# Kernel tuning notes

Hardware: AMD Instinct MI355X
Metric: run time of the kernel (lower is better)

## Reference

```python
import math
import jax, jax.numpy as jnp
import numpy as np

D_MODEL = 1024
D_STATE = 16
DT_MIN, DT_MAX, DT_INIT_FLOOR = 1e-3, 1e-1, 1e-4


def setup_inputs() -> dict:
    key = jax.random.key(0)
    ks = jax.random.split(key, 7)
    B, L, D, N = 2, 2048, D_MODEL, D_STATE
    hidden_states = jax.random.normal(ks[0], (B, L, D), dtype=jnp.float32)
    # dt init: exp(U*(log dt_max - log dt_min) + log dt_min), clamped, then log
    u = jax.random.uniform(ks[1], (D,), dtype=jnp.float32)
    dt = jnp.clip(jnp.exp(u * (math.log(DT_MAX) - math.log(DT_MIN)) + math.log(DT_MIN)), DT_INIT_FLOOR, None)
    log_dt = jnp.log(dt)
    A_real_log = jnp.log(0.5 * jnp.ones((D, N), dtype=jnp.float32))
    A_imag = jnp.broadcast_to(math.pi * jnp.arange(1, N + 1, dtype=jnp.float32)[None, :], (D, N)).copy()
    # xavier_normal std for (D, N)
    std = math.sqrt(2.0 / (D + N))
    B_re = std * jax.random.normal(ks[2], (D, N), dtype=jnp.float32)
    B_im = std * jax.random.normal(ks[3], (D, N), dtype=jnp.float32)
    C_re = std * jax.random.normal(ks[4], (D, N), dtype=jnp.float32)
    C_im = std * jax.random.normal(ks[5], (D, N), dtype=jnp.float32)
    Dparam = jnp.ones((D,), dtype=jnp.float32)
    return {"hidden_states": hidden_states, "log_dt": log_dt, "A_real_log": A_real_log,
            "A_imag": A_imag, "B_re": B_re, "B_im": B_im, "C_re": C_re, "C_im": C_im,
            "Dparam": Dparam}


def reference(hidden_states, log_dt, A_real_log, A_imag, B_re, B_im, C_re, C_im, Dparam):
    # hidden_states: (B, L, D)
    Bsz, L, Dm = hidden_states.shape
    A = -jnp.exp(A_real_log) + 1j * A_imag              # (D, N) complex64
    dt = jnp.exp(log_dt)                                 # (D,), broadcast over (B, L)
    delta = jax.nn.softplus(dt)                          # delta_softplus=True
    dA = jnp.exp(delta[:, None] * A)                     # (D, N) time-invariant discretized A
    Bc = B_re + 1j * B_im                                # (D, N)
    Cc = C_re + 1j * C_im                                # (D, N)
    dB = (delta[:, None] * Bc)                           # (D, N)

    xs = jnp.transpose(hidden_states, (1, 0, 2))         # (L, B, D)
    h0 = jnp.zeros((Bsz, Dm, A.shape[1]), dtype=A.dtype)

    def step(h, xt):
        # h: (B, D, N) complex; xt: (B, D) real
        h = dA[None] * h + dB[None] * xt[..., None].astype(h.dtype)
        y = 2.0 * jnp.real(jnp.einsum('bdn,dn->bd', h, Cc))  # complex C/B => 2*real
        return h, y

    _, ys = jax.lax.scan(step, h0, xs)                   # ys: (L, B, D)
    out = jnp.transpose(ys, (1, 0, 2)) + hidden_states * Dparam[None, None, :]
    return out
```

## Files before the change

### kernel.cpp

```cpp
#include <hip/hip_runtime.h>
#include <math.h>

namespace {
constexpr int kB = 2;
constexpr int kL = 2048;
constexpr int kD = 1024;
constexpr int kN = 16;
constexpr int kChunk = 32;
constexpr int kNC = kL / kChunk;
constexpr int kW = 24;
}

typedef float f2 __attribute__((ext_vector_type(2)));

__device__ __forceinline__ float s4_delta(float log_dt) {
  return log1pf(expf(expf(log_dt)));
}

__device__ __forceinline__ f2 s4_step(f2 g, f2 arr, f2 amp, f2 x2) {
  f2 gs = __builtin_shufflevector(g, g, 1, 0);
  f2 t = __builtin_elementwise_fma(arr, g, x2);
  return __builtin_elementwise_fma(amp, gs, t);
}

__global__ __launch_bounds__(64) void s4_window(
    const float* __restrict__ X, const float* __restrict__ log_dt,
    const float* __restrict__ A_real_log, const float* __restrict__ A_imag,
    const float* __restrict__ B_re, const float* __restrict__ B_im,
    const float* __restrict__ C_re, const float* __restrict__ C_im,
    const float* __restrict__ Dparam, float* __restrict__ Y)
{
  const int lane = threadIdx.x;
  const int bid = blockIdx.x;
  const int dblk = bid & 15;
  const int c = (bid >> 4) & (kNC - 1);
  const int b = bid >> 10;
  const int d = dblk * 64 + lane;

  const size_t base = ((size_t)b * kL + (size_t)c * kChunk) * kD + d;
  const float* xp = X + base;

  float xw[kW];
  float xo[kChunk];
  if (c > 0) {
    #pragma unroll
    for (int i = 0; i < kW; ++i) xw[i] = xp[(ptrdiff_t)(i - kW) * kD];
  }
  #pragma unroll
  for (int i = 0; i < kChunk; ++i) xo[i] = xp[(size_t)i * kD];

  const float delta = s4_delta(log_dt[d]);

  f2 arr[kN], amp[kN], cb[kN];
  {
    const float4* arl4 = reinterpret_cast<const float4*>(A_real_log + (size_t)d * kN);
    const float4* ai4  = reinterpret_cast<const float4*>(A_imag + (size_t)d * kN);
    const float4* br4  = reinterpret_cast<const float4*>(B_re + (size_t)d * kN);
    const float4* bi4  = reinterpret_cast<const float4*>(B_im + (size_t)d * kN);
    const float4* cr4  = reinterpret_cast<const float4*>(C_re + (size_t)d * kN);
    const float4* ci4  = reinterpret_cast<const float4*>(C_im + (size_t)d * kN);
    #pragma unroll
    for (int q = 0; q < 4; ++q) {
      float4 a = arl4[q];
      float4 im = ai4[q];
      float4 br = br4[q];
      float4 bi = bi4[q];
      float4 cr = cr4[q];
      float4 ci = ci4[q];
      float av[4] = {a.x, a.y, a.z, a.w};
      float iv[4] = {im.x, im.y, im.z, im.w};
      float brv[4] = {br.x, br.y, br.z, br.w};
      float biv[4] = {bi.x, bi.y, bi.z, bi.w};
      float crv[4] = {cr.x, cr.y, cr.z, cr.w};
      float civ[4] = {ci.x, ci.y, ci.z, ci.w};
      #pragma unroll
      for (int j = 0; j < 4; ++j) {
        const int n = q * 4 + j;
        float mag = expf(-delta * expf(av[j]));
        float ph = delta * iv[j];
        float are = mag * cosf(ph);
        float aim = mag * sinf(ph);
        arr[n] = (f2){are, are};
        amp[n] = (f2){-aim, aim};
        float dbre = delta * brv[j];
        float dbim = delta * biv[j];
        float cbre = 2.f * (crv[j] * dbre - civ[j] * dbim);
        float cbim = 2.f * (crv[j] * dbim + civ[j] * dbre);
        cb[n] = (f2){cbre, -cbim};
      }
    }
  }
  const float Dd = Dparam[d];

  f2 g[kN];
  #pragma unroll
  for (int n = 0; n < kN; ++n) g[n] = (f2){0.f, 0.f};

  if (c > 0) {
    #pragma unroll
    for (int t = 0; t < kW; ++t) {
      const f2 x2 = (f2){xw[t], 0.f};
      #pragma unroll
      for (int n = 0; n < kN; ++n) g[n] = s4_step(g[n], arr[n], amp[n], x2);
    }
  }

  float* yp = Y + base;
  #pragma unroll
  for (int t = 0; t < kChunk; ++t) {
    const float x = xo[t];
    const f2 x2 = (f2){x, 0.f};
    f2 ya0 = (f2){x * Dd, 0.f};
    f2 ya1 = (f2){0.f, 0.f}, ya2 = (f2){0.f, 0.f}, ya3 = (f2){0.f, 0.f};
    #pragma unroll
    for (int n = 0; n < kN; ++n) {
      g[n] = s4_step(g[n], arr[n], amp[n], x2);
      if ((n & 3) == 0)      ya0 = __builtin_elementwise_fma(cb[n], g[n], ya0);
      else if ((n & 3) == 1) ya1 = __builtin_elementwise_fma(cb[n], g[n], ya1);
      else if ((n & 3) == 2) ya2 = __builtin_elementwise_fma(cb[n], g[n], ya2);
      else                   ya3 = __builtin_elementwise_fma(cb[n], g[n], ya3);
    }
    const f2 ys = (ya0 + ya1) + (ya2 + ya3);
    yp[(size_t)t * kD] = ys.x + ys.y;
  }
}

extern "C" void kernel_launch(void* const* d_in, const int* in_sizes, int n_in,
                              void* d_out, int out_size, void* d_ws, size_t ws_size,
                              hipStream_t stream) {
  const float* X          = (const float*)d_in[0];
  const float* log_dt     = (const float*)d_in[1];
  const float* A_real_log = (const float*)d_in[2];
  const float* A_imag     = (const float*)d_in[3];
  const float* B_re       = (const float*)d_in[4];
  const float* B_im       = (const float*)d_in[5];
  const float* C_re       = (const float*)d_in[6];
  const float* C_im       = (const float*)d_in[7];
  const float* Dparam     = (const float*)d_in[8];
  float* Y = (float*)d_out;

  const int nblk = kB * kNC * (kD / 64);
  s4_window<<<nblk, 64, 0, stream>>>(X, log_dt, A_real_log, A_imag,
                                     B_re, B_im, C_re, C_im, Dparam, Y);
}
```

Baseline: 102.4 us.

## Stage input chunk with warmup window in LDS via float4 loads, double chunk length

Measured after the change: 105.8 us. +3.4%, slower.

```diff
diff --git a/kernel.cpp b/kernel.cpp
--- a/kernel.cpp
+++ b/kernel.cpp
@@ -6,9 +6,12 @@
 constexpr int kL = 2048;
 constexpr int kD = 1024;
 constexpr int kN = 16;
-constexpr int kChunk = 32;
+constexpr int kChunk = 64;
 constexpr int kNC = kL / kChunk;
 constexpr int kW = 24;
+constexpr int kDQ = 8;
+constexpr int kSlice = kD / kDQ;
+constexpr int kRows = kChunk + kW;
 }
 
 typedef float f2 __attribute__((ext_vector_type(2)));
@@ -23,31 +26,38 @@
   return __builtin_elementwise_fma(amp, gs, t);
 }
 
-__global__ __launch_bounds__(64) void s4_window(
+__global__ __launch_bounds__(128) void s4_lds(
     const float* __restrict__ X, const float* __restrict__ log_dt,
     const float* __restrict__ A_real_log, const float* __restrict__ A_imag,
     const float* __restrict__ B_re, const float* __restrict__ B_im,
     const float* __restrict__ C_re, const float* __restrict__ C_im,
     const float* __restrict__ Dparam, float* __restrict__ Y)
 {
-  const int lane = threadIdx.x;
+  __shared__ float sx[kRows * kSlice];
+
+  const int tid = threadIdx.x;
   const int bid = blockIdx.x;
-  const int dblk = bid & 15;
-  const int c = (bid >> 4) & (kNC - 1);
-  const int b = bid >> 10;
-  const int d = dblk * 64 + lane;
+  const int dq = bid & 7;
+  const int c = (bid >> 3) & (kNC - 1);
+  const int b = bid >> 8;
+  const int d = dq * kSlice + tid;
 
-  const size_t base = ((size_t)b * kL + (size_t)c * kChunk) * kD + d;
-  const float* xp = X + base;
-
-  float xw[kW];
-  float xo[kChunk];
-  if (c > 0) {
-    #pragma unroll
-    for (int i = 0; i < kW; ++i) xw[i] = xp[(ptrdiff_t)(i - kW) * kD];
+  const int woff = (c > 0) ? kW : 0;
+  const int nrows = kChunk + woff;
+  const int slot0 = kW - woff;
+  {
+    const size_t gbase = ((size_t)b * kL + (size_t)(c * kChunk - woff)) * kD
+                         + (size_t)dq * kSlice;
+    float4* s4v = reinterpret_cast<float4*>(sx);
+    const int n4 = nrows * (kSlice / 4);
+    #pragma unroll 4
+    for (int i = tid; i < n4; i += 128) {
+      const int r = i >> 5;
+      const int j = i & 31;
+      const float4* src = reinterpret_cast<const float4*>(X + gbase + (size_t)r * kD);
+      s4v[(slot0 + r) * (kSlice / 4) + j] = src[j];
+    }
   }
-  #pragma unroll
-  for (int i = 0; i < kChunk; ++i) xo[i] = xp[(size_t)i * kD];
 
   const float delta = s4_delta(log_dt[d]);
 
@@ -92,36 +102,48 @@
   }
   const float Dd = Dparam[d];
 
+  __syncthreads();
+
   f2 g[kN];
   #pragma unroll
   for (int n = 0; n < kN; ++n) g[n] = (f2){0.f, 0.f};
 
   if (c > 0) {
-    #pragma unroll
-    for (int t = 0; t < kW; ++t) {
-      const f2 x2 = (f2){xw[t], 0.f};
+    for (int tt = 0; tt < kW; tt += 8) {
+      float xg[8];
       #pragma unroll
-      for (int n = 0; n < kN; ++n) g[n] = s4_step(g[n], arr[n], amp[n], x2);
+      for (int j = 0; j < 8; ++j) xg[j] = sx[(tt + j) * kSlice + tid];
+      #pragma unroll
+      for (int j = 0; j < 8; ++j) {
+        const f2 x2 = (f2){xg[j], 0.f};
+        #pragma unroll
+        for (int n = 0; n < kN; ++n) g[n] = s4_step(g[n], arr[n], amp[n], x2);
+      }
     }
   }
 
-  float* yp = Y + base;
-  #pragma unroll
-  for (int t = 0; t < kChunk; ++t) {
-    const float x = xo[t];
-    const f2 x2 = (f2){x, 0.f};
-    f2 ya0 = (f2){x * Dd, 0.f};
-    f2 ya1 = (f2){0.f, 0.f}, ya2 = (f2){0.f, 0.f}, ya3 = (f2){0.f, 0.f};
+  float* yp = Y + ((size_t)b * kL + (size_t)c * kChunk) * kD + d;
+  for (int tt = 0; tt < kChunk; tt += 8) {
+    float xg[8];
     #pragma unroll
-    for (int n = 0; n < kN; ++n) {
-      g[n] = s4_step(g[n], arr[n], amp[n], x2);
-      if ((n & 3) == 0)      ya0 = __builtin_elementwise_fma(cb[n], g[n], ya0);
-      else if ((n & 3) == 1) ya1 = __builtin_elementwise_fma(cb[n], g[n], ya1);
-      else if ((n & 3) == 2) ya2 = __builtin_elementwise_fma(cb[n], g[n], ya2);
-      else                   ya3 = __builtin_elementwise_fma(cb[n], g[n], ya3);
+    for (int j = 0; j < 8; ++j) xg[j] = sx[(kW + tt + j) * kSlice + tid];
+    #pragma unroll
+    for (int j = 0; j < 8; ++j) {
+      const float x = xg[j];
+      const f2 x2 = (f2){x, 0.f};
+      f2 ya0 = (f2){x * Dd, 0.f};
+      f2 ya1 = (f2){0.f, 0.f}, ya2 = (f2){0.f, 0.f}, ya3 = (f2){0.f, 0.f};
+      #pragma unroll
+      for (int n = 0; n < kN; ++n) {
+        g[n] = s4_step(g[n], arr[n], amp[n], x2);
+        if ((n & 3) == 0)      ya0 = __builtin_elementwise_fma(cb[n], g[n], ya0);
+        else if ((n & 3) == 1) ya1 = __builtin_elementwise_fma(cb[n], g[n], ya1);
+        else if ((n & 3) == 2) ya2 = __builtin_elementwise_fma(cb[n], g[n], ya2);
+        else                   ya3 = __builtin_elementwise_fma(cb[n], g[n], ya3);
+      }
+      const f2 ys = (ya0 + ya1) + (ya2 + ya3);
+      yp[(size_t)(tt + j) * kD] = ys.x + ys.y;
     }
-    const f2 ys = (ya0 + ya1) + (ya2 + ya3);
-    yp[(size_t)t * kD] = ys.x + ys.y;
   }
 }
 
@@ -139,7 +161,7 @@
   const float* Dparam     = (const float*)d_in[8];
   float* Y = (float*)d_out;
 
-  const int nblk = kB * kNC * (kD / 64);
-  s4_window<<<nblk, 64, 0, stream>>>(X, log_dt, A_real_log, A_imag,
-                                     B_re, B_im, C_re, C_im, Dparam, Y);
+  const int nblk = kB * kNC * kDQ;
+  s4_lds<<<nblk, 128, 0, stream>>>(X, log_dt, A_real_log, A_imag,
+                                   B_re, B_im, C_re, C_im, Dparam, Y);
 }
```

## Replace windowed complex recurrence with precomputed 24-tap FIR convolution

Applied to the files above, without the earlier changes.

After: 92.05 us (median of 2 runs). 10.1% less time.

```diff
diff --git a/kernel.cpp b/kernel.cpp
--- a/kernel.cpp
+++ b/kernel.cpp
@@ -6,122 +6,110 @@
 constexpr int kL = 2048;
 constexpr int kD = 1024;
 constexpr int kN = 16;
-constexpr int kChunk = 32;
-constexpr int kNC = kL / kChunk;
-constexpr int kW = 24;
+constexpr int kK = 24;
+constexpr int kT = 32;
+constexpr int kHalo = kK - 1;
 }
-
-typedef float f2 __attribute__((ext_vector_type(2)));
 
 __device__ __forceinline__ float s4_delta(float log_dt) {
   return log1pf(expf(expf(log_dt)));
 }
 
-__device__ __forceinline__ f2 s4_step(f2 g, f2 arr, f2 amp, f2 x2) {
-  f2 gs = __builtin_shufflevector(g, g, 1, 0);
-  f2 t = __builtin_elementwise_fma(arr, g, x2);
-  return __builtin_elementwise_fma(amp, gs, t);
-}
-
-__global__ __launch_bounds__(64) void s4_window(
-    const float* __restrict__ X, const float* __restrict__ log_dt,
+__global__ __launch_bounds__(256) void s4_taps(
+    const float* __restrict__ log_dt,
     const float* __restrict__ A_real_log, const float* __restrict__ A_imag,
     const float* __restrict__ B_re, const float* __restrict__ B_im,
     const float* __restrict__ C_re, const float* __restrict__ C_im,
-    const float* __restrict__ Dparam, float* __restrict__ Y)
+    const float* __restrict__ Dparam, float* __restrict__ H)
 {
-  const int lane = threadIdx.x;
-  const int bid = blockIdx.x;
-  const int dblk = bid & 15;
-  const int c = (bid >> 4) & (kNC - 1);
-  const int b = bid >> 10;
-  const int d = dblk * 64 + lane;
-
-  const size_t base = ((size_t)b * kL + (size_t)c * kChunk) * kD + d;
-  const float* xp = X + base;
-
-  float xw[kW];
-  float xo[kChunk];
-  if (c > 0) {
-    #pragma unroll
-    for (int i = 0; i < kW; ++i) xw[i] = xp[(ptrdiff_t)(i - kW) * kD];
-  }
-  #pragma unroll
-  for (int i = 0; i < kChunk; ++i) xo[i] = xp[(size_t)i * kD];
+  const int tid = blockIdx.x * 256 + threadIdx.x;
+  const int d = tid & (kD - 1);
+  const int k = tid >> 10;
 
   const float delta = s4_delta(log_dt[d]);
+  const float kf = (float)k;
+  float acc = (k == 0) ? Dparam[d] : 0.f;
 
-  f2 arr[kN], amp[kN], cb[kN];
-  {
-    const float4* arl4 = reinterpret_cast<const float4*>(A_real_log + (size_t)d * kN);
-    const float4* ai4  = reinterpret_cast<const float4*>(A_imag + (size_t)d * kN);
-    const float4* br4  = reinterpret_cast<const float4*>(B_re + (size_t)d * kN);
-    const float4* bi4  = reinterpret_cast<const float4*>(B_im + (size_t)d * kN);
-    const float4* cr4  = reinterpret_cast<const float4*>(C_re + (size_t)d * kN);
-    const float4* ci4  = reinterpret_cast<const float4*>(C_im + (size_t)d * kN);
+  const float4* arl4 = reinterpret_cast<const float4*>(A_real_log + (size_t)d * kN);
+  const float4* ai4  = reinterpret_cast<const float4*>(A_imag + (size_t)d * kN);
+  const float4* br4  = reinterpret_cast<const float4*>(B_re + (size_t)d * kN);
+  const float4* bi4  = reinterpret_cast<const float4*>(B_im + (size_t)d * kN);
+  const float4* cr4  = reinterpret_cast<const float4*>(C_re + (size_t)d * kN);
+  const float4* ci4  = reinterpret_cast<const float4*>(C_im + (size_t)d * kN);
+  #pragma unroll
+  for (int q = 0; q < 4; ++q) {
+    float4 a = arl4[q];
+    float4 im = ai4[q];
+    float4 br = br4[q];
+    float4 bi = bi4[q];
+    float4 cr = cr4[q];
+    float4 ci = ci4[q];
+    float av[4] = {a.x, a.y, a.z, a.w};
+    float iv[4] = {im.x, im.y, im.z, im.w};
+    float brv[4] = {br.x, br.y, br.z, br.w};
+    float biv[4] = {bi.x, bi.y, bi.z, bi.w};
+    float crv[4] = {cr.x, cr.y, cr.z, cr.w};
+    float civ[4] = {ci.x, ci.y, ci.z, ci.w};
     #pragma unroll
-    for (int q = 0; q < 4; ++q) {
-      float4 a = arl4[q];
-      float4 im = ai4[q];
-      float4 br = br4[q];
-      float4 bi = bi4[q];
-      float4 cr = cr4[q];
-      float4 ci = ci4[q];
-      float av[4] = {a.x, a.y, a.z, a.w};
-      float iv[4] = {im.x, im.y, im.z, im.w};
-      float brv[4] = {br.x, br.y, br.z, br.w};
-      float biv[4] = {bi.x, bi.y, bi.z, bi.w};
-      float crv[4] = {cr.x, cr.y, cr.z, cr.w};
-      float civ[4] = {ci.x, ci.y, ci.z, ci.w};
-      #pragma unroll
-      for (int j = 0; j < 4; ++j) {
-        const int n = q * 4 + j;
-        float mag = expf(-delta * expf(av[j]));
-        float ph = delta * iv[j];
-        float are = mag * cosf(ph);
-        float aim = mag * sinf(ph);
-        arr[n] = (f2){are, are};
-        amp[n] = (f2){-aim, aim};
-        float dbre = delta * brv[j];
-        float dbim = delta * biv[j];
-        float cbre = 2.f * (crv[j] * dbre - civ[j] * dbim);
-        float cbim = 2.f * (crv[j] * dbim + civ[j] * dbre);
-        cb[n] = (f2){cbre, -cbim};
-      }
+    for (int j = 0; j < 4; ++j) {
+      float mag = expf(-kf * delta * expf(av[j]));
+      float ph = kf * delta * iv[j];
+      float er = mag * cosf(ph);
+      float ei = mag * sinf(ph);
+      float dbre = delta * brv[j];
+      float dbim = delta * biv[j];
+      float wre = 2.f * (crv[j] * dbre - civ[j] * dbim);
+      float wim = 2.f * (crv[j] * dbim + civ[j] * dbre);
+      acc += wre * er - wim * ei;
     }
   }
-  const float Dd = Dparam[d];
+  H[(size_t)k * kD + d] = acc;
+}
 
-  f2 g[kN];
-  #pragma unroll
-  for (int n = 0; n < kN; ++n) g[n] = (f2){0.f, 0.f};
+__global__ __launch_bounds__(256) void s4_fir(
+    const float* __restrict__ X, const float* __restrict__ H,
+    float* __restrict__ Y)
+{
+  const int lane = threadIdx.x & 63;
+  const int wid = blockIdx.x * 4 + (threadIdx.x >> 6);
+  const int dblk = wid & 15;
+  const int tile = (wid >> 4) & 63;
+  const int b = wid >> 10;
+  const int d = dblk * 64 + lane;
+  const int t0 = tile * kT;
 
-  if (c > 0) {
+  const float* xp = X + (size_t)b * kL * kD + d;
+
+  float xw[kT + kHalo];
+  if (tile > 0) {
     #pragma unroll
-    for (int t = 0; t < kW; ++t) {
-      const f2 x2 = (f2){xw[t], 0.f};
-      #pragma unroll
-      for (int n = 0; n < kN; ++n) g[n] = s4_step(g[n], arr[n], amp[n], x2);
-    }
+    for (int i = 0; i < kT + kHalo; ++i)
+      xw[i] = xp[(size_t)(t0 - kHalo + i) * kD];
+  } else {
+    #pragma unroll
+    for (int i = 0; i < kHalo; ++i) xw[i] = 0.f;
+    #pragma unroll
+    for (int i = kHalo; i < kT + kHalo; ++i)
+      xw[i] = xp[(size_t)(i - kHalo) * kD];
   }
 
-  float* yp = Y + base;
+  float h[kK];
   #pragma unroll
-  for (int t = 0; t < kChunk; ++t) {
-    const float x = xo[t];
-    const f2 x2 = (f2){x, 0.f};
-    f2 ya0 = (f2){x * Dd, 0.f};
-    f2 ya1 = (f2){0.f, 0.f}, ya2 = (f2){0.f, 0.f}, ya3 = (f2){0.f, 0.f};
+  for (int k = 0; k < kK; ++k) h[k] = H[(size_t)k * kD + d];
+
+  float* yp = Y + ((size_t)b * kL + t0) * kD + d;
+  #pragma unroll
+  for (int j = 0; j < kT; ++j) {
+    float a0 = 0.f, a1 = 0.f, a2 = 0.f, a3 = 0.f;
     #pragma unroll
-    for (int n = 0; n < kN; ++n) {
-      g[n] = s4_step(g[n], arr[n], amp[n], x2);
-      if ((n & 3) == 0)      ya0 = __builtin_elementwise_fma(cb[n], g[n], ya0);
-      else if ((n & 3) == 1) ya1 = __builtin_elementwise_fma(cb[n], g[n], ya1);
-      else if ((n & 3) == 2) ya2 = __builtin_elementwise_fma(cb[n], g[n], ya2);
-      else                   ya3 = __builtin_elementwise_fma(cb[n], g[n], ya3);
+    for (int k = 0; k < kK; ++k) {
+      const float v = xw[kHalo + j - k];
+      if ((k & 3) == 0)      a0 = fmaf(h[k], v, a0);
+      else if ((k & 3) == 1) a1 = fmaf(h[k], v, a1);
+      else if ((k & 3) == 2) a2 = fmaf(h[k], v, a2);
+      else                   a3 = fmaf(h[k], v, a3);
     }
-    const f2 ys = (ya0 + ya1) + (ya2 + ya3);
-    yp[(size_t)t * kD] = ys.x + ys.y;
+    yp[(size_t)j * kD] = (a0 + a1) + (a2 + a3);
   }
 }
 
@@ -139,7 +127,11 @@
   const float* Dparam     = (const float*)d_in[8];
   float* Y = (float*)d_out;
 
-  const int nblk = kB * kNC * (kD / 64);
-  s4_window<<<nblk, 64, 0, stream>>>(X, log_dt, A_real_log, A_imag,
-                                     B_re, B_im, C_re, C_im, Dparam, Y);
+  float* H = (float*)d_ws;
+
+  s4_taps<<<(kK * kD) / 256, 256, 0, stream>>>(
+      log_dt, A_real_log, A_imag, B_re, B_im, C_re, C_im, Dparam, H);
+
+  const int nwaves = kB * (kL / kT) * (kD / 64);
+  s4_fir<<<nwaves / 4, 256, 0, stream>>>(X, H, Y);
 }
```
